# Kernel tuning notes

Measured on AMD Instinct MI355X. Metric: run time of the kernel, lower is better.

The kernel has to match this reference:

```python
import jax, jax.numpy as jnp
import numpy as np

N_NODES = 100000
NNZ = 1600000
IN_CH = 256
OUT_CH = 64  # heads * out_channels, heads=1


def setup_inputs() -> dict:
    key = jax.random.key(0)
    k1, k2, k3, k4, k5 = jax.random.split(key, 5)
    X = jax.random.normal(k1, (N_NODES, IN_CH), dtype=jnp.float32)
    # nn.Linear(in, heads*out, bias=False) weight: [out, in]
    W_lin = jax.random.normal(k2, (OUT_CH, IN_CH), dtype=jnp.float32) * (1.0 / np.sqrt(IN_CH))
    # sparse Laplacian L in COO form
    L_rows = jax.random.randint(k3, (NNZ,), 0, N_NODES, dtype=jnp.int64)
    L_cols = jax.random.randint(k4, (NNZ,), 0, N_NODES, dtype=jnp.int64)
    L_vals = jax.random.uniform(k5, (NNZ,), dtype=jnp.float32)
    return {"g1": 0, "g2": 0, "X": X, "W_lin": W_lin,
            "L_rows": L_rows, "L_cols": L_cols, "L_vals": L_vals}


def reference(g1, g2, X, W_lin, L_rows, L_cols, L_vals):
    # dense projection: X @ W^T  -> [N, out]
    Xp = jnp.einsum('ni,oi->no', X, W_lin)
    # SpMM: Xv = L @ Xp, COO gather-scale-scatter
    gathered = L_vals[:, None] * Xp[L_cols]            # [nnz, out]
    Xv = jax.ops.segment_sum(gathered, L_rows, num_segments=N_NODES)
    return Xv
```

## Files before the change

### kernel.cpp

```cpp
#include <hip/hip_runtime.h>

#define N_IN_CH 256
#define N_OUT_CH 64
#define XPAD 264
#define BROW 128
#define NBK 1024
#define B1_E 4096
#define ECAP 4096
#define OVFCAP 65536
#define GEMM_GRID 768

typedef __attribute__((ext_vector_type(8))) short short8;
typedef __attribute__((ext_vector_type(4))) float f32x4;

__device__ inline ushort f2bf(float f) {
    unsigned u = __float_as_uint(f);
    return (ushort)((u + 0x7FFFu + ((u >> 16) & 1u)) >> 16);
}
__device__ inline float bf2f(ushort u) {
    return __uint_as_float(((unsigned)u) << 16);
}

__global__ void wbf_kernel(const float* __restrict__ W, ushort* __restrict__ Wbf) {
    int i = blockIdx.x * blockDim.x + threadIdx.x;
    if (i < N_OUT_CH * N_IN_CH) Wbf[i] = f2bf(W[i]);
}

__global__ __launch_bounds__(256) void mfma_gemm_kernel(const float* __restrict__ X,
        const ushort* __restrict__ Wbf, ushort* __restrict__ Xp, int nrows) {
    __shared__ ushort Ws[64 * XPAD];
    const int tid = threadIdx.x;

    #pragma unroll
    for (int it = 0; it < 16; ++it) {
        int f = it * 256 + tid;
        int n = f >> 6, c4 = f & 63;
        *(ushort4*)&Ws[n * XPAD + c4 * 4] = *(const ushort4*)&Wbf[n * N_IN_CH + c4 * 4];
    }
    __syncthreads();

    const int wave = tid >> 6, lane = tid & 63;
    const int ml = lane & 15, q = lane >> 4;
    const int ntiles = (nrows + 15) >> 4;
    const int nw = gridDim.x * 4;
    int t = blockIdx.x * 4 + wave;

    const ushort* wsb = &Ws[ml * XPAD + q * 8];

    float4 raw[16];

#define ISSUE_TILE(tt)                                                     \
    do {                                                                   \
        int gr_ = (tt) * 16 + ml;                                          \
        if (gr_ < nrows) {                                                 \
            const float* xr_ = X + (size_t)gr_ * N_IN_CH + q * 8;          \
            _Pragma("unroll")                                              \
            for (int kt_ = 0; kt_ < 8; ++kt_) {                            \
                raw[2 * kt_]     = *(const float4*)&xr_[kt_ * 32];         \
                raw[2 * kt_ + 1] = *(const float4*)&xr_[kt_ * 32 + 4];     \
            }                                                              \
        } else {                                                           \
            _Pragma("unroll")                                              \
            for (int i_ = 0; i_ < 16; ++i_)                                \
                raw[i_] = make_float4(0.f, 0.f, 0.f, 0.f);                 \
        }                                                                  \
    } while (0)

    if (t < ntiles) ISSUE_TILE(t);

    while (t < ntiles) {
        short8 a[8];
        #pragma unroll
        for (int kt = 0; kt < 8; ++kt) {
            float4 f0 = raw[2 * kt], f1 = raw[2 * kt + 1];
            short8 s;
            s[0] = (short)f2bf(f0.x); s[1] = (short)f2bf(f0.y);
            s[2] = (short)f2bf(f0.z); s[3] = (short)f2bf(f0.w);
            s[4] = (short)f2bf(f1.x); s[5] = (short)f2bf(f1.y);
            s[6] = (short)f2bf(f1.z); s[7] = (short)f2bf(f1.w);
            a[kt] = s;
        }
        int tn = t + nw;
        if (tn < ntiles) ISSUE_TILE(tn);

        #pragma unroll
        for (int nt = 0; nt < 4; ++nt) {
            f32x4 acc = {0.f, 0.f, 0.f, 0.f};
            #pragma unroll
            for (int kt = 0; kt < 8; ++kt) {
                short8 b = *(const short8*)&wsb[nt * 16 * XPAD + kt * 32];
                acc = __builtin_amdgcn_mfma_f32_16x16x32_bf16(a[kt], b, acc, 0, 0, 0);
            }
            #pragma unroll
            for (int reg = 0; reg < 4; ++reg) {
                int gr = t * 16 + q * 4 + reg;
                if (gr < nrows)
                    Xp[(size_t)gr * N_OUT_CH + nt * 16 + ml] = f2bf(acc[reg]);
            }
        }
        t = tn;
    }
#undef ISSUE_TILE
}

__global__ __launch_bounds__(1024) void bin_kernel(const int* __restrict__ rows,
        const int* __restrict__ cols, const float* __restrict__ vals,
        int* __restrict__ bcur, int* __restrict__ ovfcnt, int4* __restrict__ ovf,
        int2* __restrict__ colbuf, int nnz, int nb) {
    __shared__ int cnt[NBK];
    __shared__ int base[NBK];
    const int t = threadIdx.x;

    for (int i = t; i < nb; i += 1024) cnt[i] = 0;
    __syncthreads();

    const int e = blockIdx.x * B1_E + t * 4;
    int nval = nnz - e;
    if (nval > 4) nval = 4;
    if (nval < 0) nval = 0;

    int r[4], c[4]; float v[4];
    if (nval == 4) {
        int4 rr = *(const int4*)&rows[e];
        int4 cc = *(const int4*)&cols[e];
        float4 vv = *(const float4*)&vals[e];
        r[0] = rr.x; r[1] = rr.y; r[2] = rr.z; r[3] = rr.w;
        c[0] = cc.x; c[1] = cc.y; c[2] = cc.z; c[3] = cc.w;
        v[0] = vv.x; v[1] = vv.y; v[2] = vv.z; v[3] = vv.w;
    } else {
        #pragma unroll
        for (int j = 0; j < 4; ++j)
            if (j < nval) { r[j] = rows[e + j]; c[j] = cols[e + j]; v[j] = vals[e + j]; }
    }

    #pragma unroll
    for (int j = 0; j < 4; ++j)
        if (j < nval) atomicAdd(&cnt[r[j] >> 7], 1);
    __syncthreads();

    for (int i = t; i < nb; i += 1024) {
        int cn = cnt[i];
        base[i] = cn ? atomicAdd(&bcur[i], cn) : 0;
        cnt[i] = 0;
    }
    __syncthreads();

    #pragma unroll
    for (int j = 0; j < 4; ++j) {
        if (j < nval) {
            int b = r[j] >> 7;
            int pib = base[b] + atomicAdd(&cnt[b], 1);
            if (pib < ECAP) {
                int2 cv;
                cv.x = c[j] | ((r[j] & 127) << 17);
                cv.y = __float_as_int(v[j]);
                colbuf[(size_t)b * ECAP + pib] = cv;
            } else {
                int op = atomicAdd(ovfcnt, 1);
                if (op < OVFCAP) {
                    int4 o; o.x = r[j]; o.y = c[j];
                    o.z = __float_as_int(v[j]); o.w = 0;
                    ovf[op] = o;
                }
            }
        }
    }
}

__global__ __launch_bounds__(512) void bspmm_kernel(const int* __restrict__ bcur,
        const int2* __restrict__ colbuf, const ushort* __restrict__ Xp,
        float* __restrict__ out, int nrows) {
    __shared__ int2 ebuf[ECAP];
    __shared__ int rc[BROW];
    __shared__ int rb[BROW + 1];
    const int b = blockIdx.x, t = threadIdx.x;
    const int ne = min(bcur[b], ECAP);
    const int2* cb = colbuf + (size_t)b * ECAP;
    const int row0 = b * BROW;
    const int wave = t >> 6, lane = t & 63;

    if (t < BROW) rc[t] = 0;
    __syncthreads();
    for (int i = t; i < ne; i += 512)
        atomicAdd(&rc[(cb[i].x >> 17) & (BROW - 1)], 1);
    __syncthreads();
    int c0 = (t < BROW) ? rc[t] : 0;
    #pragma unroll
    for (int d = 1; d < BROW; d <<= 1) {
        int a = (t < BROW && t >= d) ? rc[t - d] : 0;
        __syncthreads();
        if (t < BROW) rc[t] += a;
        __syncthreads();
    }
    if (t < BROW) rb[t] = rc[t] - c0;
    if (t == 0) rb[BROW] = ne;
    __syncthreads();
    if (t < BROW) rc[t] = 0;
    __syncthreads();
    for (int i = t; i < ne; i += 512) {
        int2 cv = cb[i];
        int rl = (cv.x >> 17) & (BROW - 1);
        int pos = rb[rl] + atomicAdd(&rc[rl], 1);
        ebuf[pos] = cv;
    }
    __syncthreads();
    for (int r = wave; r < BROW; r += 8) {
        int gr = row0 + r;
        if (gr >= nrows) break;
        int s = rb[r], e = rb[r + 1];
        float a0 = 0.f, a1 = 0.f, a2 = 0.f, a3 = 0.f;
        int i = s;
        for (; i + 4 <= e; i += 4) {
            int2 c0v = ebuf[i], c1v = ebuf[i + 1];
            int2 c2v = ebuf[i + 2], c3v = ebuf[i + 3];
            float x0 = bf2f(Xp[(size_t)(c0v.x & 0x1FFFF) * N_OUT_CH + lane]);
            float x1 = bf2f(Xp[(size_t)(c1v.x & 0x1FFFF) * N_OUT_CH + lane]);
            float x2 = bf2f(Xp[(size_t)(c2v.x & 0x1FFFF) * N_OUT_CH + lane]);
            float x3 = bf2f(Xp[(size_t)(c3v.x & 0x1FFFF) * N_OUT_CH + lane]);
            a0 += __int_as_float(c0v.y) * x0;
            a1 += __int_as_float(c1v.y) * x1;
            a2 += __int_as_float(c2v.y) * x2;
            a3 += __int_as_float(c3v.y) * x3;
        }
        for (; i < e; ++i) {
            int2 cv = ebuf[i];
            a0 += __int_as_float(cv.y) *
                  bf2f(Xp[(size_t)(cv.x & 0x1FFFF) * N_OUT_CH + lane]);
        }
        out[(size_t)gr * N_OUT_CH + lane] = (a0 + a1) + (a2 + a3);
    }
}

__global__ __launch_bounds__(256) void ovf_kernel(const int* __restrict__ ovfcnt,
        const int4* __restrict__ ovf, const ushort* __restrict__ Xp,
        float* __restrict__ out) {
    int n = min(ovfcnt[0], OVFCAP);
    int lane = threadIdx.x & 63;
    for (int e = blockIdx.x * 4 + (threadIdx.x >> 6); e < n; e += gridDim.x * 4) {
        int4 v = ovf[e];
        atomicAdd(&out[(size_t)v.x * N_OUT_CH + lane],
                  __int_as_float(v.z) * bf2f(Xp[(size_t)v.y * N_OUT_CH + lane]));
    }
}

__global__ __launch_bounds__(256) void spmm_atomic_kernel(const int* __restrict__ rows,
        const int* __restrict__ cols, const float* __restrict__ vals,
        const ushort* __restrict__ Xp, float* __restrict__ out, int nnz) {
    int t = blockIdx.x * blockDim.x + threadIdx.x;
    int e = t >> 6;
    int c = t & 63;
    if (e < nnz) {
        atomicAdd(&out[(size_t)rows[e] * N_OUT_CH + c],
                  vals[e] * bf2f(Xp[(size_t)cols[e] * N_OUT_CH + c]));
    }
}

extern "C" void kernel_launch(void* const* d_in, const int* in_sizes, int n_in,
                              void* d_out, int out_size, void* d_ws, size_t ws_size,
                              hipStream_t stream) {
    const float* X      = (const float*)d_in[2];
    const float* W      = (const float*)d_in[3];
    const int*   L_rows = (const int*)d_in[4];
    const int*   L_cols = (const int*)d_in[5];
    const float* L_vals = (const float*)d_in[6];
    float* out = (float*)d_out;

    const int nrows = in_sizes[2] / N_IN_CH;
    const int nnz   = in_sizes[4];
    const int nb    = (nrows + BROW - 1) / BROW;

    size_t off_wbf = 0;
    size_t off_xp  = 65536;
    size_t xp_b    = (size_t)nrows * N_OUT_CH * 2;
    size_t off_bc  = off_xp + ((xp_b + 15) & ~(size_t)15);
    size_t off_ov  = off_bc + (((size_t)(nb + 1) * 4 + 15) & ~(size_t)15);
    size_t off_cv  = off_ov + (size_t)OVFCAP * 16;
    size_t need    = off_cv + (size_t)nb * ECAP * 8;

    ushort* Wbf = (ushort*)((char*)d_ws + off_wbf);
    ushort* Xp  = (ushort*)((char*)d_ws + off_xp);

    wbf_kernel<<<(N_OUT_CH * N_IN_CH + 255) / 256, 256, 0, stream>>>(W, Wbf);
    {
        int ntiles = (nrows + 15) >> 4;
        int grid = GEMM_GRID;
        int maxg = (ntiles + 3) / 4;
        if (grid > maxg) grid = maxg;
        mfma_gemm_kernel<<<grid, 256, 0, stream>>>(X, Wbf, Xp, nrows);
    }

    if (ws_size >= need && nb <= NBK) {
        int*  bcur   = (int*)((char*)d_ws + off_bc);
        int*  ovfcnt = bcur + nb;
        int4* ovf    = (int4*)((char*)d_ws + off_ov);
        int2* colbuf = (int2*)((char*)d_ws + off_cv);

        hipMemsetAsync(bcur, 0, (size_t)(nb + 1) * 4, stream);
        bin_kernel<<<(nnz + B1_E - 1) / B1_E, 1024, 0, stream>>>(L_rows, L_cols, L_vals,
                bcur, ovfcnt, ovf, colbuf, nnz, nb);
        bspmm_kernel<<<nb, 512, 0, stream>>>(bcur, colbuf, Xp, out, nrows);
        ovf_kernel<<<16, 256, 0, stream>>>(ovfcnt, ovf, Xp, out);
    } else {
        hipMemsetAsync(d_out, 0, (size_t)out_size * sizeof(float), stream);
        long long total = (long long)nnz * 64;
        spmm_atomic_kernel<<<(int)((total + 255) / 256), 256, 0, stream>>>(
            L_rows, L_cols, L_vals, Xp, out, nnz);
    }
}
```

Before: 257.1 us.

## Fuse weight conversion and counter zeroing into GEMM, rebalance binning and SpMM loops

The separate weight-to-bf16 kernel is removed; the GEMM now converts fp32 weights into shared memory directly, and block 0 zeroes the bin counters so the memset is dropped. The binning kernel moves to 512 threads, each handling 8 edges. The SpMM phase changes from one wave per row to one wave per contiguous 16-row segment, streaming 8 gathers at a time and flushing output on row change, with a separate pass writing zeros for empty rows. This removes two launches and should give the gathers more memory-level parallelism, at the cost of every GEMM block redoing the weight conversion and of branchy per-edge row-change checks.

```diff
diff --git a/kernel.cpp b/kernel.cpp
--- a/kernel.cpp
+++ b/kernel.cpp
@@ -5,6 +5,7 @@
 #define XPAD 264
 #define BROW 128
 #define NBK 1024
+#define B1_T 512
 #define B1_E 4096
 #define ECAP 4096
 #define OVFCAP 65536
@@ -21,21 +22,24 @@
     return __uint_as_float(((unsigned)u) << 16);
 }
 
-__global__ void wbf_kernel(const float* __restrict__ W, ushort* __restrict__ Wbf) {
-    int i = blockIdx.x * blockDim.x + threadIdx.x;
-    if (i < N_OUT_CH * N_IN_CH) Wbf[i] = f2bf(W[i]);
-}
-
 __global__ __launch_bounds__(256) void mfma_gemm_kernel(const float* __restrict__ X,
-        const ushort* __restrict__ Wbf, ushort* __restrict__ Xp, int nrows) {
+        const float* __restrict__ W, ushort* __restrict__ Xp, int nrows,
+        int* __restrict__ zbuf, int nzero) {
     __shared__ ushort Ws[64 * XPAD];
     const int tid = threadIdx.x;
+
+    if (blockIdx.x == 0) {
+        for (int i = tid; i < nzero; i += 256) zbuf[i] = 0;
+    }
 
     #pragma unroll
     for (int it = 0; it < 16; ++it) {
         int f = it * 256 + tid;
         int n = f >> 6, c4 = f & 63;
-        *(ushort4*)&Ws[n * XPAD + c4 * 4] = *(const ushort4*)&Wbf[n * N_IN_CH + c4 * 4];
+        float4 w = *(const float4*)&W[n * N_IN_CH + c4 * 4];
+        ushort4 u;
+        u.x = f2bf(w.x); u.y = f2bf(w.y); u.z = f2bf(w.z); u.w = f2bf(w.w);
+        *(ushort4*)&Ws[n * XPAD + c4 * 4] = u;
     }
     __syncthreads();
 
@@ -103,7 +107,7 @@
 #undef ISSUE_TILE
 }
 
-__global__ __launch_bounds__(1024) void bin_kernel(const int* __restrict__ rows,
+__global__ __launch_bounds__(B1_T) void bin_kernel(const int* __restrict__ rows,
         const int* __restrict__ cols, const float* __restrict__ vals,
         int* __restrict__ bcur, int* __restrict__ ovfcnt, int4* __restrict__ ovf,
         int2* __restrict__ colbuf, int nnz, int nb) {
@@ -111,34 +115,34 @@
     __shared__ int base[NBK];
     const int t = threadIdx.x;
 
-    for (int i = t; i < nb; i += 1024) cnt[i] = 0;
-    __syncthreads();
-
-    const int e = blockIdx.x * B1_E + t * 4;
+    for (int i = t; i < nb; i += B1_T) cnt[i] = 0;
+    __syncthreads();
+
+    const int e = blockIdx.x * B1_E + t * 8;
     int nval = nnz - e;
-    if (nval > 4) nval = 4;
+    if (nval > 8) nval = 8;
     if (nval < 0) nval = 0;
 
-    int r[4], c[4]; float v[4];
-    if (nval == 4) {
-        int4 rr = *(const int4*)&rows[e];
-        int4 cc = *(const int4*)&cols[e];
-        float4 vv = *(const float4*)&vals[e];
-        r[0] = rr.x; r[1] = rr.y; r[2] = rr.z; r[3] = rr.w;
-        c[0] = cc.x; c[1] = cc.y; c[2] = cc.z; c[3] = cc.w;
-        v[0] = vv.x; v[1] = vv.y; v[2] = vv.z; v[3] = vv.w;
+    int r[8], c[8]; float v[8];
+    if (nval == 8) {
+        *(int4*)&r[0] = *(const int4*)&rows[e];
+        *(int4*)&r[4] = *(const int4*)&rows[e + 4];
+        *(int4*)&c[0] = *(const int4*)&cols[e];
+        *(int4*)&c[4] = *(const int4*)&cols[e + 4];
+        *(float4*)&v[0] = *(const float4*)&vals[e];
+        *(float4*)&v[4] = *(const float4*)&vals[e + 4];
     } else {
         #pragma unroll
-        for (int j = 0; j < 4; ++j)
+        for (int j = 0; j < 8; ++j)
             if (j < nval) { r[j] = rows[e + j]; c[j] = cols[e + j]; v[j] = vals[e + j]; }
     }
 
     #pragma unroll
-    for (int j = 0; j < 4; ++j)
+    for (int j = 0; j < 8; ++j)
         if (j < nval) atomicAdd(&cnt[r[j] >> 7], 1);
     __syncthreads();
 
-    for (int i = t; i < nb; i += 1024) {
+    for (int i = t; i < nb; i += B1_T) {
         int cn = cnt[i];
         base[i] = cn ? atomicAdd(&bcur[i], cn) : 0;
         cnt[i] = 0;
@@ -146,7 +150,7 @@
     __syncthreads();
 
     #pragma unroll
-    for (int j = 0; j < 4; ++j) {
+    for (int j = 0; j < 8; ++j) {
         if (j < nval) {
             int b = r[j] >> 7;
             int pib = base[b] + atomicAdd(&cnt[b], 1);
@@ -204,30 +208,47 @@
         ebuf[pos] = cv;
     }
     __syncthreads();
-    for (int r = wave; r < BROW; r += 8) {
-        int gr = row0 + r;
-        if (gr >= nrows) break;
-        int s = rb[r], e = rb[r + 1];
-        float a0 = 0.f, a1 = 0.f, a2 = 0.f, a3 = 0.f;
-        int i = s;
-        for (; i + 4 <= e; i += 4) {
-            int2 c0v = ebuf[i], c1v = ebuf[i + 1];
-            int2 c2v = ebuf[i + 2], c3v = ebuf[i + 3];
-            float x0 = bf2f(Xp[(size_t)(c0v.x & 0x1FFFF) * N_OUT_CH + lane]);
-            float x1 = bf2f(Xp[(size_t)(c1v.x & 0x1FFFF) * N_OUT_CH + lane]);
-            float x2 = bf2f(Xp[(size_t)(c2v.x & 0x1FFFF) * N_OUT_CH + lane]);
-            float x3 = bf2f(Xp[(size_t)(c3v.x & 0x1FFFF) * N_OUT_CH + lane]);
-            a0 += __int_as_float(c0v.y) * x0;
-            a1 += __int_as_float(c1v.y) * x1;
-            a2 += __int_as_float(c2v.y) * x2;
-            a3 += __int_as_float(c3v.y) * x3;
-        }
-        for (; i < e; ++i) {
-            int2 cv = ebuf[i];
-            a0 += __int_as_float(cv.y) *
-                  bf2f(Xp[(size_t)(cv.x & 0x1FFFF) * N_OUT_CH + lane]);
-        }
-        out[(size_t)gr * N_OUT_CH + lane] = (a0 + a1) + (a2 + a3);
+
+    const int r0 = wave * 16;
+    const int s = rb[r0], e = rb[r0 + 16];
+    float accv = 0.f;
+    int cur = -1;
+    int i = s;
+    for (; i + 8 <= e; i += 8) {
+        int2 cv[8];
+        #pragma unroll
+        for (int j = 0; j < 8; ++j) cv[j] = ebuf[i + j];
+        float x[8];
+        #pragma unroll
+        for (int j = 0; j < 8; ++j)
+            x[j] = bf2f(Xp[(size_t)(cv[j].x & 0x1FFFF) * N_OUT_CH + lane]);
+        #pragma unroll
+        for (int j = 0; j < 8; ++j) {
+            int rl = (cv[j].x >> 17) & (BROW - 1);
+            if (rl != cur) {
+                if (cur >= 0) out[(size_t)(row0 + cur) * N_OUT_CH + lane] = accv;
+                cur = rl; accv = 0.f;
+            }
+            accv += __int_as_float(cv[j].y) * x[j];
+        }
+    }
+    for (; i < e; ++i) {
+        int2 cv = ebuf[i];
+        int rl = (cv.x >> 17) & (BROW - 1);
+        if (rl != cur) {
+            if (cur >= 0) out[(size_t)(row0 + cur) * N_OUT_CH + lane] = accv;
+            cur = rl; accv = 0.f;
+        }
+        accv += __int_as_float(cv.y) *
+                bf2f(Xp[(size_t)(cv.x & 0x1FFFF) * N_OUT_CH + lane]);
+    }
+    if (cur >= 0) out[(size_t)(row0 + cur) * N_OUT_CH + lane] = accv;
+
+    for (int r = r0; r < r0 + 16; ++r) {
+        if (rb[r] == rb[r + 1]) {
+            int gr = row0 + r;
+            if (gr < nrows) out[(size_t)gr * N_OUT_CH + lane] = 0.f;
+        }
     }
 }
 
@@ -269,34 +290,32 @@
     const int nnz   = in_sizes[4];
     const int nb    = (nrows + BROW - 1) / BROW;
 
-    size_t off_wbf = 0;
-    size_t off_xp  = 65536;
+    size_t off_xp  = 0;
     size_t xp_b    = (size_t)nrows * N_OUT_CH * 2;
     size_t off_bc  = off_xp + ((xp_b + 15) & ~(size_t)15);
     size_t off_ov  = off_bc + (((size_t)(nb + 1) * 4 + 15) & ~(size_t)15);
     size_t off_cv  = off_ov + (size_t)OVFCAP * 16;
     size_t need    = off_cv + (size_t)nb * ECAP * 8;
 
-    ushort* Wbf = (ushort*)((char*)d_ws + off_wbf);
-    ushort* Xp  = (ushort*)((char*)d_ws + off_xp);
-
-    wbf_kernel<<<(N_OUT_CH * N_IN_CH + 255) / 256, 256, 0, stream>>>(W, Wbf);
+    ushort* Xp = (ushort*)((char*)d_ws + off_xp);
+    const bool binned = (ws_size >= need && nb <= NBK);
+    int* bcur = (int*)((char*)d_ws + off_bc);
+
     {
         int ntiles = (nrows + 15) >> 4;
         int grid = GEMM_GRID;
         int maxg = (ntiles + 3) / 4;
         if (grid > maxg) grid = maxg;
-        mfma_gemm_kernel<<<grid, 256, 0, stream>>>(X, Wbf, Xp, nrows);
-    }
-
-    if (ws_size >= need && nb <= NBK) {
-        int*  bcur   = (int*)((char*)d_ws + off_bc);
+        mfma_gemm_kernel<<<grid, 256, 0, stream>>>(X, W, Xp, nrows,
+                binned ? bcur : (int*)d_ws, binned ? nb + 1 : 0);
+    }
+
+    if (binned) {
         int*  ovfcnt = bcur + nb;
         int4* ovf    = (int4*)((char*)d_ws + off_ov);
         int2* colbuf = (int2*)((char*)d_ws + off_cv);
 
-        hipMemsetAsync(bcur, 0, (size_t)(nb + 1) * 4, stream);
-        bin_kernel<<<(nnz + B1_E - 1) / B1_E, 1024, 0, stream>>>(L_rows, L_cols, L_vals,
+        bin_kernel<<<(nnz + B1_E - 1) / B1_E, B1_T, 0, stream>>>(L_rows, L_cols, L_vals,
                 bcur, ovfcnt, ovf, colbuf, nnz, nb);
         bspmm_kernel<<<nb, 512, 0, stream>>>(bcur, colbuf, Xp, out, nrows);
         ovf_kernel<<<16, 256, 0, stream>>>(ovfcnt, ovf, Xp, out);
```

Result: faster. 250.1 us (-2.7%).
